# Kernel optimization log

Measured on AMD Instinct MI355X. Metric: run time of the kernel, lower is better.

The kernel has to match this reference:

```python
import jax, jax.numpy as jnp
import numpy as np

K = 5          # number of spline bins
B = 5.0        # tail bound
HIDDEN = 8
MIN_W = 1e-3; MIN_H = 1e-3; MIN_D = 1e-3  # RQS defaults (Durkan et al.)


def setup_inputs() -> dict:
    n, d = 32768, 64
    L = d - 1
    P = 3 * K - 1
    ks = jax.random.split(jax.random.key(0), 8)
    x = jax.random.normal(ks[0], (n, d), jnp.float32) * 2.0
    init_param = jax.random.uniform(ks[1], (P,), jnp.float32, -0.5, 0.5)
    # ragged first layers: layer l (predicts dim l+1) sees x[:, :l+1]; zero-pad to width L
    mask = (jnp.arange(L)[None, :] <= jnp.arange(L)[:, None]).astype(jnp.float32)
    W1 = jax.random.normal(ks[2], (L, L, HIDDEN), jnp.float32) * 0.2 * mask[:, :, None]
    b1 = jax.random.normal(ks[3], (L, HIDDEN), jnp.float32) * 0.1
    W2 = jax.random.normal(ks[4], (L, HIDDEN, HIDDEN), jnp.float32) * 0.2
    b2 = jax.random.normal(ks[5], (L, HIDDEN), jnp.float32) * 0.1
    W3 = jax.random.normal(ks[6], (L, HIDDEN, P), jnp.float32) * 0.2
    b3 = jax.random.normal(ks[7], (L, P), jnp.float32) * 0.1
    return {"x": x, "init_param": init_param, "W1": W1, "b1": b1,
            "W2": W2, "b2": b2, "W3": W3, "b3": b3}


def _rqs(xf, Wu, Hu, Du):
    # xf: (M,), Wu/Hu: (M,K), Du: (M,K-1) -- vectorized unconstrained RQS, forward
    inside = (xf >= -B) & (xf <= B)
    const = float(np.log(np.exp(1.0 - MIN_D) - 1.0))
    Dpad = jnp.pad(Du, ((0, 0), (1, 1)), constant_values=const)

    widths = MIN_W + (1.0 - MIN_W * K) * jax.nn.softmax(Wu, axis=-1)
    cumw = jnp.pad(jnp.cumsum(widths, -1), ((0, 0), (1, 0)))
    cumw = 2.0 * B * cumw - B
    cumw = cumw.at[:, 0].set(-B).at[:, -1].set(B)
    widths = cumw[:, 1:] - cumw[:, :-1]

    heights = MIN_H + (1.0 - MIN_H * K) * jax.nn.softmax(Hu, axis=-1)
    cumh = jnp.pad(jnp.cumsum(heights, -1), ((0, 0), (1, 0)))
    cumh = 2.0 * B * cumh - B
    cumh = cumh.at[:, 0].set(-B).at[:, -1].set(B)
    heights = cumh[:, 1:] - cumh[:, :-1]

    derivs = MIN_D + jax.nn.softplus(Dpad)  # (M, K+1)

    xc = jnp.clip(xf, -B, B)
    idx = jnp.clip(jnp.sum(xc[:, None] >= cumw, axis=-1) - 1, 0, K - 1)
    take = lambda a: jnp.take_along_axis(a, idx[:, None], axis=-1)[:, 0]

    icw, ibw = take(cumw), take(widths)
    ich, ih = take(cumh), take(heights)
    idl = take(heights / widths)
    idv = take(derivs)
    idvp1 = take(derivs[:, 1:])

    theta = (xc - icw) / ibw
    tmt = theta * (1.0 - theta)
    num = ih * (idl * theta * theta + idv * tmt)
    den = idl + (idv + idvp1 - 2.0 * idl) * tmt
    out = ich + num / den
    dnum = idl * idl * (idvp1 * theta * theta + 2.0 * idl * tmt + idv * (1.0 - theta) ** 2)
    ld = jnp.log(dnum) - 2.0 * jnp.log(den)
    return jnp.where(inside, out, xf), jnp.where(inside, ld, 0.0)


def reference(x, init_param, W1, b1, W2, b2, W3, b3):
    n, d = x.shape
    L = d - 1
    P = 3 * K - 1
    # mask re-applied so padded W1 entries are exactly inert (ragged Linear(i, hidden))
    mask = (jnp.arange(L)[None, :] <= jnp.arange(L)[:, None]).astype(x.dtype)
    h = jnp.tanh(jnp.einsum('nj,ljh->lnh', x[:, :L], W1 * mask[:, :, None]) + b1[:, None, :])
    h = jnp.tanh(jnp.einsum('lnh,lhg->lng', h, W2) + b2[:, None, :])
    out = jnp.einsum('lng,lgp->lnp', h, W3) + b3[:, None, :]      # (L, n, P)
    p0 = jnp.broadcast_to(init_param, (1, n, P))                  # dim 0 uses init_param
    params = jnp.concatenate([p0, out], axis=0).reshape(d * n, P)  # dim-major, matches Ws layout
    Wu, Hu, Du = params[:, :K], params[:, K:2 * K], params[:, 2 * K:]
    xf = x.T.reshape(-1)  # x.transpose(0,1).flatten()
    zs, lds = _rqs(xf, Wu, Hu, Du)
    # NOTE: faithfully replicates the original's reshape of the dim-major flat
    # vector directly to (n, d) (as in the torch source).
    return zs.reshape(n, d), lds.reshape(n, d).sum(axis=1)
```

## Files before the change

### kernel.cpp

```cpp
#include <hip/hip_runtime.h>
#include <hip/hip_bf16.h>
#include <math.h>

#define KK 5
#define Bc 5.0f
#define NN 32768
#define DD 64
#define LL 63
#define PP 14
#define MIN_Wc 0.001f
#define MIN_Hc 0.001f
#define MIN_Dc 0.001f

typedef float f4 __attribute__((ext_vector_type(4)));
typedef float f32x4 __attribute__((ext_vector_type(4)));
typedef short short8 __attribute__((ext_vector_type(8)));

__device__ __forceinline__ float rcp_fast(float v)  { return __builtin_amdgcn_rcpf(v); }
__device__ __forceinline__ float exp_fast(float v)  { return __expf(v); }
__device__ __forceinline__ float log_fast(float v)  { return __logf(v); }
__device__ __forceinline__ float tanh_fast(float v) {
    float e = exp_fast(2.0f * v);
    return 1.0f - 2.0f * rcp_fast(e + 1.0f);
}
__device__ __forceinline__ float softplus_fast(float v) {
    return (v > 15.0f) ? v : log_fast(1.0f + exp_fast(v));
}
__device__ __forceinline__ ushort to_bf16u(float v) {
    __hip_bfloat16 b = __float2bfloat16(v);
    return *(ushort*)&b;
}

__global__ __launch_bounds__(256) void pack_b1(const float* __restrict__ W1,
                                               ushort* __restrict__ Bp) {
    int id = blockIdx.x * 256 + threadIdx.x;
    int n = id >> 6, k = id & 63;
    float v = 0.f;
    if (n < 504 && k < 63) {
        int l = n >> 3, h = n & 7;
        v = W1[(l * 63 + k) * 8 + h];
    }
    Bp[id] = to_bf16u(v);
}

__device__ __forceinline__ short8 pack_a(f4 v0, f4 v1) {
    short8 a;
    a[0] = (short)to_bf16u(v0.x); a[1] = (short)to_bf16u(v0.y);
    a[2] = (short)to_bf16u(v0.z); a[3] = (short)to_bf16u(v0.w);
    a[4] = (short)to_bf16u(v1.x); a[5] = (short)to_bf16u(v1.y);
    a[6] = (short)to_bf16u(v1.z); a[7] = (short)to_bf16u(v1.w);
    return a;
}

__global__ __launch_bounds__(256) void fused_kernel(
    const float* __restrict__ x, const float* __restrict__ init_param,
    const ushort* __restrict__ Bp, const float* __restrict__ b1,
    const float* __restrict__ W2, const float* __restrict__ b2,
    const float* __restrict__ W3, const float* __restrict__ b3,
    float* __restrict__ out)
{
    __shared__ float xs[64 * 65];
    __shared__ ushort h1c[2][64 * 72];
    const int tid = threadIdx.x;
    const int s0 = blockIdx.x * 64;
    const int y  = blockIdx.y;

    for (int q = tid; q < 64 * 64; q += 256) {
        int r = q >> 6, c = q & 63;
        xs[r * 65 + c] = x[(size_t)(s0 + r) * 64 + c];
    }

    const int lane = tid & 63, wave = tid >> 6;
    const int ln = lane & 15, qg = lane >> 4;
    const int m0 = wave * 16;

    short8 a0, a1;
    {
        const float* xr = x + (size_t)(s0 + m0 + ln) * 64 + qg * 8;
        a0 = pack_a(*(const f4*)xr, *(const f4*)(xr + 4));
        if (y) a1 = pack_a(*(const f4*)(xr + 32), *(const f4*)(xr + 36));
        else   a1 = a0;
    }

    int buf = 0;
    #pragma unroll 1
    for (int c = 0; c < 4; ++c) {
        const int gc = y * 4 + c;

        #pragma unroll
        for (int nt = 0; nt < 4; ++nt) {
            int ncol = gc * 64 + nt * 16 + ln;
            const short8* bp8 = (const short8*)(Bp + ncol * 64 + qg * 8);
            f32x4 acc = {0.f, 0.f, 0.f, 0.f};
            acc = __builtin_amdgcn_mfma_f32_16x16x32_bf16(a0, bp8[0], acc, 0, 0, 0);
            if (y) acc = __builtin_amdgcn_mfma_f32_16x16x32_bf16(a1, bp8[4], acc, 0, 0, 0);
            float bias = (ncol < 504) ? b1[ncol] : 0.f;
            #pragma unroll
            for (int r = 0; r < 4; ++r) {
                float v = tanh_fast(acc[r] + bias);
                h1c[buf][(m0 + qg * 4 + r) * 72 + nt * 16 + ln] = to_bf16u(v);
            }
        }
        __syncthreads();

        #pragma unroll 1
        for (int it = 0; it < 2; ++it) {
            int idx = wave * 2 + it;
            int dd = (gc == 7 && idx == 7) ? 0 : gc * 8 + 1 + idx;
            dd = __builtin_amdgcn_readfirstlane(dd);

            float p[PP];
            if (dd == 0) {
                #pragma unroll
                for (int i = 0; i < PP; ++i) p[i] = init_param[i];
            } else {
                const int l = dd - 1;
                const int dl = l - gc * 8;
                uint4 hv = *(const uint4*)&h1c[buf][lane * 72 + dl * 8];
                float h1f[8];
                h1f[0] = __uint_as_float(hv.x << 16);
                h1f[1] = __uint_as_float(hv.x & 0xFFFF0000u);
                h1f[2] = __uint_as_float(hv.y << 16);
                h1f[3] = __uint_as_float(hv.y & 0xFFFF0000u);
                h1f[4] = __uint_as_float(hv.z << 16);
                h1f[5] = __uint_as_float(hv.z & 0xFFFF0000u);
                h1f[6] = __uint_as_float(hv.w << 16);
                h1f[7] = __uint_as_float(hv.w & 0xFFFF0000u);

                float h2[8];
                #pragma unroll
                for (int g = 0; g < 8; ++g) h2[g] = b2[l * 8 + g];
                #pragma unroll
                for (int h = 0; h < 8; ++h) {
                    #pragma unroll
                    for (int g = 0; g < 8; ++g)
                        h2[g] = fmaf(h1f[h], W2[l * 64 + h * 8 + g], h2[g]);
                }
                #pragma unroll
                for (int g = 0; g < 8; ++g) h2[g] = tanh_fast(h2[g]);

                #pragma unroll
                for (int q = 0; q < PP; ++q) p[q] = b3[l * PP + q];
                #pragma unroll
                for (int g = 0; g < 8; ++g) {
                    #pragma unroll
                    for (int q = 0; q < PP; ++q)
                        p[q] = fmaf(h2[g], W3[(l * 8 + g) * PP + q], p[q]);
                }
            }

            const float xf = xs[lane * 65 + dd];

            float wmax = p[0];
            #pragma unroll
            for (int i = 1; i < KK; ++i) wmax = fmaxf(wmax, p[i]);
            float we[KK]; float wsum = 0.f;
            #pragma unroll
            for (int i = 0; i < KK; ++i) { we[i] = exp_fast(p[i] - wmax); wsum += we[i]; }
            const float wnorm = (1.0f - MIN_Wc * KK) * rcp_fast(wsum);
            float cumw[KK + 1], wdt[KK];
            cumw[0] = -Bc;
            float acw = 0.f;
            #pragma unroll
            for (int i = 0; i < KK; ++i) { acw += MIN_Wc + wnorm * we[i]; cumw[i + 1] = 2.f * Bc * acw - Bc; }
            cumw[KK] = Bc;
            #pragma unroll
            for (int i = 0; i < KK; ++i) wdt[i] = cumw[i + 1] - cumw[i];

            float hmax = p[KK];
            #pragma unroll
            for (int i = 1; i < KK; ++i) hmax = fmaxf(hmax, p[KK + i]);
            float he[KK]; float hsum = 0.f;
            #pragma unroll
            for (int i = 0; i < KK; ++i) { he[i] = exp_fast(p[KK + i] - hmax); hsum += he[i]; }
            const float hnorm = (1.0f - MIN_Hc * KK) * rcp_fast(hsum);
            float cumh[KK + 1], hgt[KK];
            cumh[0] = -Bc;
            float ach = 0.f;
            #pragma unroll
            for (int i = 0; i < KK; ++i) { ach += MIN_Hc + hnorm * he[i]; cumh[i + 1] = 2.f * Bc * ach - Bc; }
            cumh[KK] = Bc;
            #pragma unroll
            for (int i = 0; i < KK; ++i) hgt[i] = cumh[i + 1] - cumh[i];

            float derivs[KK + 1];
            derivs[0] = 1.0f;
            derivs[KK] = 1.0f;
            #pragma unroll
            for (int i = 0; i < KK - 1; ++i) derivs[i + 1] = MIN_Dc + softplus_fast(p[2 * KK + i]);

            const float xc = fminf(fmaxf(xf, -Bc), Bc);

            float icw = cumw[0], ibw = wdt[0], ich = cumh[0], ih = hgt[0];
            float idv = derivs[0], idvp1 = derivs[1];
            #pragma unroll
            for (int i = 1; i < KK; ++i) {
                bool cc = xc >= cumw[i];
                icw   = cc ? cumw[i]       : icw;
                ibw   = cc ? wdt[i]        : ibw;
                ich   = cc ? cumh[i]       : ich;
                ih    = cc ? hgt[i]        : ih;
                idv   = cc ? derivs[i]     : idv;
                idvp1 = cc ? derivs[i + 1] : idvp1;
            }

            const float ibw_r = rcp_fast(ibw);
            const float idl = ih * ibw_r;
            const float theta = (xc - icw) * ibw_r;
            const float omt = 1.0f - theta;
            const float tmt = theta * omt;
            const float num = ih * (idl * theta * theta + idv * tmt);
            const float den = idl + (idv + idvp1 - 2.0f * idl) * tmt;
            const float outv = ich + num * rcp_fast(den);
            const float dnum = idl * idl * (idvp1 * theta * theta + 2.0f * idl * tmt + idv * omt * omt);
            const float ld = log_fast(dnum) - 2.0f * log_fast(den);

            const bool inside = (xf >= -Bc) && (xf <= Bc);
            const float z = inside ? outv : xf;
            float ldv = inside ? ld : 0.0f;

            out[dd * NN + s0 + lane] = z;

            #pragma unroll
            for (int off = 32; off > 0; off >>= 1) ldv += __shfl_down(ldv, off);
            if (lane == 0) out[NN * DD + dd * (NN / 64) + blockIdx.x] = ldv;
        }
        buf ^= 1;
    }
}

extern "C" void kernel_launch(void* const* d_in, const int* in_sizes, int n_in,
                              void* d_out, int out_size, void* d_ws, size_t ws_size,
                              hipStream_t stream) {
    const float* x          = (const float*)d_in[0];
    const float* init_param = (const float*)d_in[1];
    const float* W1         = (const float*)d_in[2];
    const float* b1         = (const float*)d_in[3];
    const float* W2         = (const float*)d_in[4];
    const float* b2         = (const float*)d_in[5];
    const float* W3         = (const float*)d_in[6];
    const float* b3         = (const float*)d_in[7];
    float* out = (float*)d_out;

    ushort* Bp = (ushort*)d_ws;

    pack_b1<<<128, 256, 0, stream>>>(W1, Bp);
    fused_kernel<<<dim3(512, 2), 256, 0, stream>>>(x, init_param, Bp, b1,
                                                   W2, b2, W3, b3, out);
}
```

Baseline: 117.1 us.

## Split dims across four y-blocks, drop x smem staging and chunk loop

The grid's y dimension grows from 2 to 4, so each block handles 16 output dims in one pass instead of four chunks of 8 with double-buffered h1. The x tile is no longer staged in shared memory; each lane loads its 4 needed x values straight from global memory. Launch bounds now request 8 blocks per CU. This cuts shared memory per block and removes the per-chunk barriers, raising occupancy and parallelism. In exchange, per-lane x loads are strided (uncoalesced) and x rows are reread by more blocks.

Result: no change. 116.2 us (-0.7%).

```diff
diff --git a/kernel.cpp b/kernel.cpp
--- a/kernel.cpp
+++ b/kernel.cpp
@@ -52,180 +52,175 @@
     return a;
 }
 
-__global__ __launch_bounds__(256) void fused_kernel(
+#define H1S 136
+__global__ __launch_bounds__(256, 8) void fused_kernel(
     const float* __restrict__ x, const float* __restrict__ init_param,
     const ushort* __restrict__ Bp, const float* __restrict__ b1,
     const float* __restrict__ W2, const float* __restrict__ b2,
     const float* __restrict__ W3, const float* __restrict__ b3,
     float* __restrict__ out)
 {
-    __shared__ float xs[64 * 65];
-    __shared__ ushort h1c[2][64 * 72];
+    __shared__ ushort h1c[64 * H1S];
     const int tid = threadIdx.x;
     const int s0 = blockIdx.x * 64;
     const int y  = blockIdx.y;
-
-    for (int q = tid; q < 64 * 64; q += 256) {
-        int r = q >> 6, c = q & 63;
-        xs[r * 65 + c] = x[(size_t)(s0 + r) * 64 + c];
-    }
-
-    const int lane = tid & 63, wave = tid >> 6;
+    const int lane = tid & 63;
+    const int wave = __builtin_amdgcn_readfirstlane(tid >> 6);
     const int ln = lane & 15, qg = lane >> 4;
     const int m0 = wave * 16;
+
+    float xv[4];
+    #pragma unroll
+    for (int it = 0; it < 4; ++it) {
+        int idx = wave * 4 + it;
+        int dd = (y == 3 && idx == 15) ? 0 : y * 16 + 1 + idx;
+        xv[it] = x[(size_t)(s0 + lane) * 64 + dd];
+    }
 
     short8 a0, a1;
     {
         const float* xr = x + (size_t)(s0 + m0 + ln) * 64 + qg * 8;
         a0 = pack_a(*(const f4*)xr, *(const f4*)(xr + 4));
-        if (y) a1 = pack_a(*(const f4*)(xr + 32), *(const f4*)(xr + 36));
-        else   a1 = a0;
-    }
-
-    int buf = 0;
+        a1 = (y >= 2) ? pack_a(*(const f4*)(xr + 32), *(const f4*)(xr + 36)) : a0;
+    }
+
+    #pragma unroll
+    for (int nt = 0; nt < 8; ++nt) {
+        int ncol = y * 128 + nt * 16 + ln;
+        const short8* bp8 = (const short8*)(Bp + ncol * 64 + qg * 8);
+        f32x4 acc = {0.f, 0.f, 0.f, 0.f};
+        acc = __builtin_amdgcn_mfma_f32_16x16x32_bf16(a0, bp8[0], acc, 0, 0, 0);
+        if (y >= 2)
+            acc = __builtin_amdgcn_mfma_f32_16x16x32_bf16(a1, bp8[4], acc, 0, 0, 0);
+        float bias = (ncol < 504) ? b1[ncol] : 0.f;
+        #pragma unroll
+        for (int r = 0; r < 4; ++r) {
+            float v = tanh_fast(acc[r] + bias);
+            h1c[(m0 + qg * 4 + r) * H1S + nt * 16 + ln] = to_bf16u(v);
+        }
+    }
+    __syncthreads();
+
     #pragma unroll 1
-    for (int c = 0; c < 4; ++c) {
-        const int gc = y * 4 + c;
-
-        #pragma unroll
-        for (int nt = 0; nt < 4; ++nt) {
-            int ncol = gc * 64 + nt * 16 + ln;
-            const short8* bp8 = (const short8*)(Bp + ncol * 64 + qg * 8);
-            f32x4 acc = {0.f, 0.f, 0.f, 0.f};
-            acc = __builtin_amdgcn_mfma_f32_16x16x32_bf16(a0, bp8[0], acc, 0, 0, 0);
-            if (y) acc = __builtin_amdgcn_mfma_f32_16x16x32_bf16(a1, bp8[4], acc, 0, 0, 0);
-            float bias = (ncol < 504) ? b1[ncol] : 0.f;
-            #pragma unroll
-            for (int r = 0; r < 4; ++r) {
-                float v = tanh_fast(acc[r] + bias);
-                h1c[buf][(m0 + qg * 4 + r) * 72 + nt * 16 + ln] = to_bf16u(v);
+    for (int it = 0; it < 4; ++it) {
+        int idx = wave * 4 + it;
+        int dd = (y == 3 && idx == 15) ? 0 : y * 16 + 1 + idx;
+        dd = __builtin_amdgcn_readfirstlane(dd);
+        const float xf = xv[it];
+
+        float p[PP];
+        if (dd == 0) {
+            #pragma unroll
+            for (int i = 0; i < PP; ++i) p[i] = init_param[i];
+        } else {
+            const int l = dd - 1;
+            const int dl = l - y * 16;
+            uint4 hv = *(const uint4*)&h1c[lane * H1S + dl * 8];
+            float h1f[8];
+            h1f[0] = __uint_as_float(hv.x << 16);
+            h1f[1] = __uint_as_float(hv.x & 0xFFFF0000u);
+            h1f[2] = __uint_as_float(hv.y << 16);
+            h1f[3] = __uint_as_float(hv.y & 0xFFFF0000u);
+            h1f[4] = __uint_as_float(hv.z << 16);
+            h1f[5] = __uint_as_float(hv.z & 0xFFFF0000u);
+            h1f[6] = __uint_as_float(hv.w << 16);
+            h1f[7] = __uint_as_float(hv.w & 0xFFFF0000u);
+
+            float h2[8];
+            #pragma unroll
+            for (int g = 0; g < 8; ++g) h2[g] = b2[l * 8 + g];
+            #pragma unroll
+            for (int h = 0; h < 8; ++h) {
+                #pragma unroll
+                for (int g = 0; g < 8; ++g)
+                    h2[g] = fmaf(h1f[h], W2[l * 64 + h * 8 + g], h2[g]);
+            }
+            #pragma unroll
+            for (int g = 0; g < 8; ++g) h2[g] = tanh_fast(h2[g]);
+
+            #pragma unroll
+            for (int q = 0; q < PP; ++q) p[q] = b3[l * PP + q];
+            #pragma unroll
+            for (int g = 0; g < 8; ++g) {
+                #pragma unroll
+                for (int q = 0; q < PP; ++q)
+                    p[q] = fmaf(h2[g], W3[(l * 8 + g) * PP + q], p[q]);
             }
         }
-        __syncthreads();
-
-        #pragma unroll 1
-        for (int it = 0; it < 2; ++it) {
-            int idx = wave * 2 + it;
-            int dd = (gc == 7 && idx == 7) ? 0 : gc * 8 + 1 + idx;
-            dd = __builtin_amdgcn_readfirstlane(dd);
-
-            float p[PP];
-            if (dd == 0) {
-                #pragma unroll
-                for (int i = 0; i < PP; ++i) p[i] = init_param[i];
-            } else {
-                const int l = dd - 1;
-                const int dl = l - gc * 8;
-                uint4 hv = *(const uint4*)&h1c[buf][lane * 72 + dl * 8];
-                float h1f[8];
-                h1f[0] = __uint_as_float(hv.x << 16);
-                h1f[1] = __uint_as_float(hv.x & 0xFFFF0000u);
-                h1f[2] = __uint_as_float(hv.y << 16);
-                h1f[3] = __uint_as_float(hv.y & 0xFFFF0000u);
-                h1f[4] = __uint_as_float(hv.z << 16);
-                h1f[5] = __uint_as_float(hv.z & 0xFFFF0000u);
-                h1f[6] = __uint_as_float(hv.w << 16);
-                h1f[7] = __uint_as_float(hv.w & 0xFFFF0000u);
-
-                float h2[8];
-                #pragma unroll
-                for (int g = 0; g < 8; ++g) h2[g] = b2[l * 8 + g];
-                #pragma unroll
-                for (int h = 0; h < 8; ++h) {
-                    #pragma unroll
-                    for (int g = 0; g < 8; ++g)
-                        h2[g] = fmaf(h1f[h], W2[l * 64 + h * 8 + g], h2[g]);
-                }
-                #pragma unroll
-                for (int g = 0; g < 8; ++g) h2[g] = tanh_fast(h2[g]);
-
-                #pragma unroll
-                for (int q = 0; q < PP; ++q) p[q] = b3[l * PP + q];
-                #pragma unroll
-                for (int g = 0; g < 8; ++g) {
-                    #pragma unroll
-                    for (int q = 0; q < PP; ++q)
-                        p[q] = fmaf(h2[g], W3[(l * 8 + g) * PP + q], p[q]);
-                }
-            }
-
-            const float xf = xs[lane * 65 + dd];
-
-            float wmax = p[0];
-            #pragma unroll
-            for (int i = 1; i < KK; ++i) wmax = fmaxf(wmax, p[i]);
-            float we[KK]; float wsum = 0.f;
-            #pragma unroll
-            for (int i = 0; i < KK; ++i) { we[i] = exp_fast(p[i] - wmax); wsum += we[i]; }
-            const float wnorm = (1.0f - MIN_Wc * KK) * rcp_fast(wsum);
-            float cumw[KK + 1], wdt[KK];
-            cumw[0] = -Bc;
-            float acw = 0.f;
-            #pragma unroll
-            for (int i = 0; i < KK; ++i) { acw += MIN_Wc + wnorm * we[i]; cumw[i + 1] = 2.f * Bc * acw - Bc; }
-            cumw[KK] = Bc;
-            #pragma unroll
-            for (int i = 0; i < KK; ++i) wdt[i] = cumw[i + 1] - cumw[i];
-
-            float hmax = p[KK];
-            #pragma unroll
-            for (int i = 1; i < KK; ++i) hmax = fmaxf(hmax, p[KK + i]);
-            float he[KK]; float hsum = 0.f;
-            #pragma unroll
-            for (int i = 0; i < KK; ++i) { he[i] = exp_fast(p[KK + i] - hmax); hsum += he[i]; }
-            const float hnorm = (1.0f - MIN_Hc * KK) * rcp_fast(hsum);
-            float cumh[KK + 1], hgt[KK];
-            cumh[0] = -Bc;
-            float ach = 0.f;
-            #pragma unroll
-            for (int i = 0; i < KK; ++i) { ach += MIN_Hc + hnorm * he[i]; cumh[i + 1] = 2.f * Bc * ach - Bc; }
-            cumh[KK] = Bc;
-            #pragma unroll
-            for (int i = 0; i < KK; ++i) hgt[i] = cumh[i + 1] - cumh[i];
-
-            float derivs[KK + 1];
-            derivs[0] = 1.0f;
-            derivs[KK] = 1.0f;
-            #pragma unroll
-            for (int i = 0; i < KK - 1; ++i) derivs[i + 1] = MIN_Dc + softplus_fast(p[2 * KK + i]);
-
-            const float xc = fminf(fmaxf(xf, -Bc), Bc);
-
-            float icw = cumw[0], ibw = wdt[0], ich = cumh[0], ih = hgt[0];
-            float idv = derivs[0], idvp1 = derivs[1];
-            #pragma unroll
-            for (int i = 1; i < KK; ++i) {
-                bool cc = xc >= cumw[i];
-                icw   = cc ? cumw[i]       : icw;
-                ibw   = cc ? wdt[i]        : ibw;
-                ich   = cc ? cumh[i]       : ich;
-                ih    = cc ? hgt[i]        : ih;
-                idv   = cc ? derivs[i]     : idv;
-                idvp1 = cc ? derivs[i + 1] : idvp1;
-            }
-
-            const float ibw_r = rcp_fast(ibw);
-            const float idl = ih * ibw_r;
-            const float theta = (xc - icw) * ibw_r;
-            const float omt = 1.0f - theta;
-            const float tmt = theta * omt;
-            const float num = ih * (idl * theta * theta + idv * tmt);
-            const float den = idl + (idv + idvp1 - 2.0f * idl) * tmt;
-            const float outv = ich + num * rcp_fast(den);
-            const float dnum = idl * idl * (idvp1 * theta * theta + 2.0f * idl * tmt + idv * omt * omt);
-            const float ld = log_fast(dnum) - 2.0f * log_fast(den);
-
-            const bool inside = (xf >= -Bc) && (xf <= Bc);
-            const float z = inside ? outv : xf;
-            float ldv = inside ? ld : 0.0f;
-
-            out[dd * NN + s0 + lane] = z;
-
-            #pragma unroll
-            for (int off = 32; off > 0; off >>= 1) ldv += __shfl_down(ldv, off);
-            if (lane == 0) out[NN * DD + dd * (NN / 64) + blockIdx.x] = ldv;
+
+        float wmax = p[0];
+        #pragma unroll
+        for (int i = 1; i < KK; ++i) wmax = fmaxf(wmax, p[i]);
+        float we[KK]; float wsum = 0.f;
+        #pragma unroll
+        for (int i = 0; i < KK; ++i) { we[i] = exp_fast(p[i] - wmax); wsum += we[i]; }
+        const float wnorm = (1.0f - MIN_Wc * KK) * rcp_fast(wsum);
+        float cumw[KK + 1], wdt[KK];
+        cumw[0] = -Bc;
+        float acw = 0.f;
+        #pragma unroll
+        for (int i = 0; i < KK; ++i) { acw += MIN_Wc + wnorm * we[i]; cumw[i + 1] = 2.f * Bc * acw - Bc; }
+        cumw[KK] = Bc;
+        #pragma unroll
+        for (int i = 0; i < KK; ++i) wdt[i] = cumw[i + 1] - cumw[i];
+
+        float hmax = p[KK];
+        #pragma unroll
+        for (int i = 1; i < KK; ++i) hmax = fmaxf(hmax, p[KK + i]);
+        float he[KK]; float hsum = 0.f;
+        #pragma unroll
+        for (int i = 0; i < KK; ++i) { he[i] = exp_fast(p[KK + i] - hmax); hsum += he[i]; }
+        const float hnorm = (1.0f - MIN_Hc * KK) * rcp_fast(hsum);
+        float cumh[KK + 1], hgt[KK];
+        cumh[0] = -Bc;
+        float ach = 0.f;
+        #pragma unroll
+        for (int i = 0; i < KK; ++i) { ach += MIN_Hc + hnorm * he[i]; cumh[i + 1] = 2.f * Bc * ach - Bc; }
+        cumh[KK] = Bc;
+        #pragma unroll
+        for (int i = 0; i < KK; ++i) hgt[i] = cumh[i + 1] - cumh[i];
+
+        float derivs[KK + 1];
+        derivs[0] = 1.0f;
+        derivs[KK] = 1.0f;
+        #pragma unroll
+        for (int i = 0; i < KK - 1; ++i) derivs[i + 1] = MIN_Dc + softplus_fast(p[2 * KK + i]);
+
+        const float xc = fminf(fmaxf(xf, -Bc), Bc);
+
+        float icw = cumw[0], ibw = wdt[0], ich = cumh[0], ih = hgt[0];
+        float idv = derivs[0], idvp1 = derivs[1];
+        #pragma unroll
+        for (int i = 1; i < KK; ++i) {
+            bool cc = xc >= cumw[i];
+            icw   = cc ? cumw[i]       : icw;
+            ibw   = cc ? wdt[i]        : ibw;
+            ich   = cc ? cumh[i]       : ich;
+            ih    = cc ? hgt[i]        : ih;
+            idv   = cc ? derivs[i]     : idv;
+            idvp1 = cc ? derivs[i + 1] : idvp1;
         }
-        buf ^= 1;
+
+        const float ibw_r = rcp_fast(ibw);
+        const float idl = ih * ibw_r;
+        const float theta = (xc - icw) * ibw_r;
+        const float omt = 1.0f - theta;
+        const float tmt = theta * omt;
+        const float num = ih * (idl * theta * theta + idv * tmt);
+        const float den = idl + (idv + idvp1 - 2.0f * idl) * tmt;
+        const float outv = ich + num * rcp_fast(den);
+        const float dnum = idl * idl * (idvp1 * theta * theta + 2.0f * idl * tmt + idv * omt * omt);
+        const float ld = log_fast(dnum) - 2.0f * log_fast(den);
+
+        const bool inside = (xf >= -Bc) && (xf <= Bc);
+        const float z = inside ? outv : xf;
+        float ldv = inside ? ld : 0.0f;
+
+        out[dd * NN + s0 + lane] = z;
+
+        #pragma unroll
+        for (int off = 32; off > 0; off >>= 1) ldv += __shfl_down(ldv, off);
+        if (lane == 0) out[NN * DD + dd * (NN / 64) + blockIdx.x] = ldv;
     }
 }
 
@@ -245,6 +240,6 @@
     ushort* Bp = (ushort*)d_ws;
 
     pack_b1<<<128, 256, 0, stream>>>(W1, Bp);
-    fused_kernel<<<dim3(512, 2), 256, 0, stream>>>(x, init_param, Bp, b1,
+    fused_kernel<<<dim3(512, 4), 256, 0, stream>>>(x, init_param, Bp, b1,
                                                    W2, b2, W3, b3, out);
 }
```
